# Optimization experiments

Measured on AMD Instinct MI355X. Metric: run time of the kernel, lower is better.

## Reference

```python
import jax, jax.numpy as jnp
import numpy as np

B, TE, TD, D = 8, 2048, 2048, 256

def setup_inputs() -> dict:
    key = jax.random.key(0)
    k1, k2 = jax.random.split(key)
    encoder_outputs = jax.random.normal(k1, (B, TE, D), dtype=jnp.float32)
    decoder_outputs = jax.random.normal(k2, (B, TD, D), dtype=jnp.float32)
    return {"encoder_outputs": encoder_outputs, "decoder_outputs": decoder_outputs}

def reference(encoder_outputs, decoder_outputs):
    # luong_score[b,e,t] = sum_d enc[b,e,d] * dec[b,t,d]   (batch_dot with dec transposed)
    luong_score = jnp.einsum('bed,btd->bet', encoder_outputs, decoder_outputs)
    # softmax over encoder-time axis (axis=1)
    luong_score = jax.nn.softmax(luong_score, axis=1)
    # original does expand_dims + broadcast-multiply + sum over axis=1;
    # same math as a contraction over e: context[b,t,d] = sum_e score[b,e,t]*enc[b,e,d]
    encoder_vector = jnp.einsum('bet,bed->btd', luong_score, encoder_outputs)
    return jnp.concatenate([decoder_outputs, encoder_vector], axis=-1)
```

## Files before the change

kernel.cpp:

```cpp
#include <hip/hip_runtime.h>

typedef _Float16 f16;
typedef _Float16 f16x4 __attribute__((ext_vector_type(4)));
typedef _Float16 f16x8 __attribute__((ext_vector_type(8)));
typedef float    f32x4 __attribute__((ext_vector_type(4)));

#define NB   8
#define TE   2048
#define TD   2048
#define DIM  256
#define NSPLIT 2
#define LOG2E 1.44269504088896340736f

#define AS1(p) ((const __attribute__((address_space(1))) void*)(p))
#define AS3(p) ((__attribute__((address_space(3))) void*)(p))

__global__ __launch_bounds__(256) void prep_kernel(const float* __restrict__ enc,
                                                   f16* __restrict__ ench,
                                                   f16* __restrict__ enct) {
    __shared__ f16 tile[64][72];
    int b  = blockIdx.z;
    int e0 = blockIdx.x * 64;
    int d0 = blockIdx.y * 64;
    int tid = threadIdx.x;
    {
        int e  = tid >> 2;
        int dg = (tid & 3) * 16;
        const float* p = enc + ((size_t)b * TE + e0 + e) * DIM + d0 + dg;
        float4 v0 = *(const float4*)(p);
        float4 v1 = *(const float4*)(p + 4);
        float4 v2 = *(const float4*)(p + 8);
        float4 v3 = *(const float4*)(p + 12);
        f16x8 o0, o1;
        o0[0]=(f16)v0.x; o0[1]=(f16)v0.y; o0[2]=(f16)v0.z; o0[3]=(f16)v0.w;
        o0[4]=(f16)v1.x; o0[5]=(f16)v1.y; o0[6]=(f16)v1.z; o0[7]=(f16)v1.w;
        o1[0]=(f16)v2.x; o1[1]=(f16)v2.y; o1[2]=(f16)v2.z; o1[3]=(f16)v2.w;
        o1[4]=(f16)v3.x; o1[5]=(f16)v3.y; o1[6]=(f16)v3.z; o1[7]=(f16)v3.w;
        *(f16x8*)&tile[e][dg]     = o0;
        *(f16x8*)&tile[e][dg + 8] = o1;
        f16* hp = ench + ((size_t)b * TE + e0 + e) * DIM + d0 + dg;
        *(f16x8*)(hp)     = o0;
        *(f16x8*)(hp + 8) = o1;
    }
    __syncthreads();
    {
        int d  = tid >> 2;
        int eg = (tid & 3) * 16;
        f16x8 o0, o1;
        #pragma unroll
        for (int ii = 0; ii < 8; ii++) o0[ii] = tile[eg + ii][d];
        #pragma unroll
        for (int ii = 0; ii < 8; ii++) o1[ii] = tile[eg + 8 + ii][d];
        f16* qp = enct + ((size_t)b * DIM + d0 + d) * TE + e0 + eg;
        *(f16x8*)(qp)     = o0;
        *(f16x8*)(qp + 8) = o1;
    }
}

#define LDS_NAT0 0
#define LDS_NAT1 16384
#define LDS_TR0  32768
#define LDS_TR1  49152
#define LDS_P    65536

__global__ __launch_bounds__(256, 2) void attn_kernel(
        const float* __restrict__ dec32,
        const f16*  __restrict__ enc_h,
        const f16*  __restrict__ enc_t,
        float* __restrict__ out,
        f16*   __restrict__ ctxp,
        float* __restrict__ m_arr,
        float* __restrict__ l_arr,
        int nsplit) {
    __shared__ char lds[75776];
    const int tid  = threadIdx.x;
    const int lane = tid & 63;
    const int wave = tid >> 6;
    const int th   = wave >> 1;
    const int dh   = wave & 1;
    const int tcol = lane & 15;
    const int q    = lane >> 4;

    int xb, b, z, iters, e_base;
    if (nsplit == NSPLIT) {
        int fid = blockIdx.x + 32 * (blockIdx.y + 8 * blockIdx.z);
        int c = fid & 7, j = fid >> 3;
        xb = j & 31;
        int g = c * 2 + (j >> 5);
        b = g & 7; z = g >> 3;
        iters  = 32;
        e_base = z * 1024;
    } else { xb = blockIdx.x; b = blockIdx.y; z = 0; iters = 64; e_base = 0; }
    const int  t0    = xb * 64;
    const bool heavy = (dh == (xb & 1));

    const f16* enc_b  = enc_h + (size_t)b * TE * DIM;
    const f16* enct_b = enc_t + (size_t)b * DIM * TE;

    const int e00 = tid >> 5, cs0 = tid & 31;
    const int nat_g0 = e00 * DIM + (cs0 ^ (e00 & 7)) * 8;
    const int d00 = tid >> 2, c00 = tid & 3;
    const int tr_g0  = d00 * TE + (c00 ^ ((d00 >> 1) & 3)) * 8;
    const int l0     = wave * 1024;

    #pragma unroll
    for (int i = 0; i < 4; i++)
        __builtin_amdgcn_global_load_lds(AS1(enc_b + (size_t)e_base * DIM + nat_g0 + i * 2048),
                                         AS3(lds + LDS_NAT0 + l0 + i * 4096), 16, 0, 0);
    #pragma unroll
    for (int i = 0; i < 4; i++)
        __builtin_amdgcn_global_load_lds(AS1(enc_b + (size_t)(e_base + 32) * DIM + nat_g0 + i * 2048),
                                         AS3(lds + LDS_NAT1 + l0 + i * 4096), 16, 0, 0);
    #pragma unroll
    for (int i = 0; i < 4; i++)
        __builtin_amdgcn_global_load_lds(AS1(enct_b + e_base + tr_g0 + i * 64 * TE),
                                         AS3(lds + LDS_TR0 + l0 + i * 4096), 16, 0, 0);

    if (nsplit == 1) {
        const float* dp = dec32 + ((size_t)b * TD + t0) * DIM;
        float*       op = out   + ((size_t)b * TD + t0) * 512;
        #pragma unroll
        for (int i = 0; i < 16; i++) {
            int idx = i * 256 + tid;
            int t = idx >> 6, c = idx & 63;
            float4 v = *(const float4*)(dp + t * DIM + c * 4);
            *(float4*)(op + t * 512 + c * 4) = v;
        }
    }

    f16x8 qf[2][8];
    if (heavy) {
        const float* qp = dec32 + ((size_t)b * TD + t0 + th * 32) * DIM;
        #pragma unroll
        for (int tn = 0; tn < 2; tn++)
            #pragma unroll
            for (int ks = 0; ks < 8; ks++) {
                const float* p = qp + (size_t)(tn * 16 + tcol) * DIM + ks * 32 + q * 8;
                float4 u = *(const float4*)(p);
                float4 v = *(const float4*)(p + 4);
                f16x8 o;
                o[0]=(f16)u.x; o[1]=(f16)u.y; o[2]=(f16)u.z; o[3]=(f16)u.w;
                o[4]=(f16)v.x; o[5]=(f16)v.y; o[6]=(f16)v.z; o[7]=(f16)v.w;
                qf[tn][ks] = o;
            }
    }

    f16x8 ones;
    #pragma unroll
    for (int j = 0; j < 8; j++) ones[j] = (f16)1.0f;

    const f32x4 zero4 = {0.f, 0.f, 0.f, 0.f};
    float m_[2] = {-INFINITY, -INFINITY};
    f32x4 lsum[2] = {zero4, zero4};
    f32x4 ctx[8][2];
    #pragma unroll
    for (int dm = 0; dm < 8; dm++)
        #pragma unroll
        for (int tn = 0; tn < 2; tn++) ctx[dm][tn] = zero4;

    const int e7 = tcol & 7;

    __syncthreads();

    for (int it = 0; it < iters; it++) {
        const int natc = (it & 1) ? LDS_NAT1 : LDS_NAT0;
        const int trc  = (it & 1) ? LDS_TR1  : LDS_TR0;
        char* pb = lds + LDS_P + ((it & 1) ? 5120 : 0) + th * 2560;

        if (heavy) {
            f32x4 st[2][2];
            #pragma unroll
            for (int mt = 0; mt < 2; mt++)
                #pragma unroll
                for (int tn = 0; tn < 2; tn++) st[mt][tn] = zero4;
            #pragma unroll
            for (int ks = 0; ks < 8; ks++) {
                #pragma unroll
                for (int mt = 0; mt < 2; mt++) {
                    int e = mt * 16 + tcol;
                    f16x8 af = *(const f16x8*)(lds + natc + e * 512 + (((ks << 2) | q) ^ e7) * 16);
                    #pragma unroll
                    for (int tn = 0; tn < 2; tn++)
                        st[mt][tn] = __builtin_amdgcn_mfma_f32_16x16x32_f16(af, qf[tn][ks], st[mt][tn], 0, 0, 0);
                }
            }
            #pragma unroll
            for (int tn = 0; tn < 2; tn++) {
                float mx = fmaxf(fmaxf(fmaxf(st[0][tn][0], st[0][tn][1]), fmaxf(st[0][tn][2], st[0][tn][3])),
                                 fmaxf(fmaxf(st[1][tn][0], st[1][tn][1]), fmaxf(st[1][tn][2], st[1][tn][3])));
                mx = fmaxf(mx, __shfl_xor(mx, 16, 64));
                mx = fmaxf(mx, __shfl_xor(mx, 32, 64));
                float mn = fmaxf(m_[tn], mx);
                bool bumped = mn > m_[tn];
                float al = __builtin_amdgcn_exp2f((m_[tn] - mn) * LOG2E);
                m_[tn] = mn;
                char* prow = pb + (tn * 16 + tcol) * 80;
                #pragma unroll
                for (int mt = 0; mt < 2; mt++) {
                    f16x4 pv;
                    #pragma unroll
                    for (int r = 0; r < 4; r++)
                        pv[r] = (f16)__builtin_amdgcn_exp2f((st[mt][tn][r] - mn) * LOG2E);
                    *(f16x4*)(prow + mt * 32 + q * 8) = pv;
                }
                if (q == 0) *(float*)(prow + 72) = al;
                if (__any(bumped)) {
                    lsum[tn][0] *= al; lsum[tn][1] *= al; lsum[tn][2] *= al; lsum[tn][3] *= al;
                    #pragma unroll
                    for (int dm = 0; dm < 8; dm++) {
                        ctx[dm][tn][0] *= al; ctx[dm][tn][1] *= al;
                        ctx[dm][tn][2] *= al; ctx[dm][tn][3] *= al;
                    }
                }
            }
        }

        __syncthreads();

        if (it + 1 < iters) {
            const int trn = (it & 1) ? LDS_TR0 : LDS_TR1;
            const int e1  = e_base + (it + 1) * 32;
            #pragma unroll
            for (int i = 0; i < 4; i++)
                __builtin_amdgcn_global_load_lds(AS1(enct_b + e1 + tr_g0 + i * 64 * TE),
                                                 AS3(lds + trn + l0 + i * 4096), 16, 0, 0);
        }
        if (it + 2 < iters) {
            const int e2 = e_base + (it + 2) * 32;
            #pragma unroll
            for (int i = 0; i < 4; i++)
                __builtin_amdgcn_global_load_lds(AS1(enc_b + (size_t)e2 * DIM + nat_g0 + i * 2048),
                                                 AS3(lds + natc + l0 + i * 4096), 16, 0, 0);
        }

        if (!heavy) {
            #pragma unroll
            for (int tn = 0; tn < 2; tn++) {
                float al = *(const float*)(pb + (tn * 16 + tcol) * 80 + 72);
                if (__any(al < 1.0f)) {
                    lsum[tn][0] *= al; lsum[tn][1] *= al; lsum[tn][2] *= al; lsum[tn][3] *= al;
                    #pragma unroll
                    for (int dm = 0; dm < 8; dm++) {
                        ctx[dm][tn][0] *= al; ctx[dm][tn][1] *= al;
                        ctx[dm][tn][2] *= al; ctx[dm][tn][3] *= al;
                    }
                }
            }
        }

        f16x8 pf[2];
        #pragma unroll
        for (int tn = 0; tn < 2; tn++)
            pf[tn] = *(const f16x8*)(pb + (tn * 16 + tcol) * 80 + q * 16);
        #pragma unroll
        for (int tn = 0; tn < 2; tn++)
            lsum[tn] = __builtin_amdgcn_mfma_f32_16x16x32_f16(ones, pf[tn], lsum[tn], 0, 0, 0);
        #pragma unroll
        for (int dm = 0; dm < 8; dm++) {
            int drow = dh * 128 + dm * 16 + tcol;
            f16x8 af = *(const f16x8*)(lds + trc + drow * 64 + (q ^ ((tcol >> 1) & 3)) * 16);
            #pragma unroll
            for (int tn = 0; tn < 2; tn++)
                ctx[dm][tn] = __builtin_amdgcn_mfma_f32_16x16x32_f16(af, pf[tn], ctx[dm][tn], 0, 0, 0);
        }
    }

    if (nsplit > 1) {
        size_t rowbase = (size_t)(z * NB + b) * TD + t0 + th * 32;
        #pragma unroll
        for (int tn = 0; tn < 2; tn++) {
            float inv = 1.0f / lsum[tn][0];
            size_t rb = (rowbase + tn * 16 + tcol) * DIM + dh * 128;
            #pragma unroll
            for (int dm = 0; dm < 8; dm++) {
                f16x4 cv;
                #pragma unroll
                for (int r = 0; r < 4; r++) cv[r] = (f16)(ctx[dm][tn][r] * inv);
                *(f16x4*)(ctxp + rb + dm * 16 + q * 4) = cv;
            }
        }
        if (heavy && lane < 16) {
            int mi = (z * NB + b) * TD + t0 + th * 32 + lane;
            #pragma unroll
            for (int tn = 0; tn < 2; tn++) {
                m_arr[mi + tn * 16] = m_[tn];
                l_arr[mi + tn * 16] = lsum[tn][0];
            }
        }
    } else {
        float* ob = out + ((size_t)b * TD + t0 + th * 32) * 512 + 256 + dh * 128;
        #pragma unroll
        for (int tn = 0; tn < 2; tn++) {
            float inv = 1.0f / lsum[tn][0];
            #pragma unroll
            for (int dm = 0; dm < 8; dm++)
                #pragma unroll
                for (int r = 0; r < 4; r++)
                    ob[(size_t)(tn * 16 + tcol) * 512 + dm * 16 + q * 4 + r] = ctx[dm][tn][r] * inv;
        }
    }
}

__global__ __launch_bounds__(256) void combine_kernel(const float* __restrict__ dec32,
        const f16* __restrict__ ctxp, const float* __restrict__ m_arr,
        const float* __restrict__ l_arr, float* __restrict__ out) {
    int idx  = blockIdx.x * 256 + threadIdx.x;
    int trow = idx >> 5;
    int dg   = (idx & 31) * 8;
    float m0[NSPLIT], l0[NSPLIT], M = -INFINITY;
    #pragma unroll
    for (int s = 0; s < NSPLIT; s++) {
        m0[s] = m_arr[s * (NB * TD) + trow];
        l0[s] = l_arr[s * (NB * TD) + trow];
        M = fmaxf(M, m0[s]);
    }
    float L = 0.f, w[NSPLIT];
    #pragma unroll
    for (int s = 0; s < NSPLIT; s++) {
        w[s] = __builtin_amdgcn_exp2f((m0[s] - M) * LOG2E) * l0[s];
        L += w[s];
    }
    float invL = 1.0f / L;
    float acc[8] = {0.f,0.f,0.f,0.f,0.f,0.f,0.f,0.f};
    #pragma unroll
    for (int s = 0; s < NSPLIT; s++) {
        f16x8 v = *(const f16x8*)(ctxp + ((size_t)s * (NB * TD) + trow) * DIM + dg);
        float ws = w[s] * invL;
        #pragma unroll
        for (int j = 0; j < 8; j++) acc[j] += ws * (float)v[j];
    }
    float4 d0 = *(const float4*)(dec32 + (size_t)trow * DIM + dg);
    float4 d1 = *(const float4*)(dec32 + (size_t)trow * DIM + dg + 4);
    float* ob = out + (size_t)trow * 512;
    *(float4*)(ob + dg)     = d0;
    *(float4*)(ob + dg + 4) = d1;
    float4 c0, c1;
    c0.x=acc[0]; c0.y=acc[1]; c0.z=acc[2]; c0.w=acc[3];
    c1.x=acc[4]; c1.y=acc[5]; c1.z=acc[6]; c1.w=acc[7];
    *(float4*)(ob + 256 + dg)     = c0;
    *(float4*)(ob + 256 + dg + 4) = c1;
}

extern "C" void kernel_launch(void* const* d_in, const int* in_sizes, int n_in,
                              void* d_out, int out_size, void* d_ws, size_t ws_size,
                              hipStream_t stream) {
    (void)in_sizes; (void)n_in;
    const float* enc = (const float*)d_in[0];
    const float* dec = (const float*)d_in[1];
    float* out = (float*)d_out;

    const size_t HB    = (size_t)NB * TE * DIM * 2;
    const size_t CTXPB = (size_t)NSPLIT * NB * TD * DIM * 2;
    const size_t MLB   = (size_t)NSPLIT * NB * TD * 4;
    const size_t NEED2 = 2 * HB + CTXPB + 2 * MLB;
    const size_t NEED1 = 2 * HB;

    if (ws_size < NEED1) {
        hipMemsetAsync(d_out, 0, (size_t)out_size * sizeof(float), stream);
        return;
    }
    int nsplit = (ws_size >= NEED2) ? NSPLIT : 1;

    f16*   enc_h = (f16*)d_ws;
    f16*   enc_t = (f16*)((char*)d_ws + HB);
    f16*   ctxp  = (f16*)((char*)d_ws + 2 * HB);
    float* m_arr = (float*)((char*)d_ws + 2 * HB + CTXPB);
    float* l_arr = (float*)((char*)d_ws + 2 * HB + CTXPB + MLB);

    prep_kernel<<<dim3(32, 4, 8), 256, 0, stream>>>(enc, enc_h, enc_t);
    attn_kernel<<<dim3(32, 8, nsplit), 256, 0, stream>>>(dec, enc_h, enc_t, out,
                                                         ctxp, m_arr, l_arr, nsplit);
    if (nsplit == NSPLIT)
        combine_kernel<<<2048, 256, 0, stream>>>(dec, ctxp, m_arr, l_arr, out);
}
```

Baseline: 150.8 us.

## Drop transposed encoder copy, split work by e-halves, use three-way split

The prep kernel now only converts the encoder to fp16 and no longer writes a transposed copy. The attention kernel stages a single natural-layout tile per step and reads it both for QK and, through strided scalar LDS reads, as the transposed operand for PV. Each wave pair now splits the encoder rows instead of the feature dimension, exchanging row maxima and sums through LDS with an extra barrier per step. The split is raised to three with three blocks per CU, and the nsplit=1 fallback is removed. This saves the transpose traffic and LDS space, at the cost of scalar gathers for PV, extra syncs and more combine traffic.

```diff
diff --git a/kernel.cpp b/kernel.cpp
--- a/kernel.cpp
+++ b/kernel.cpp
@@ -9,127 +9,67 @@
 #define TE   2048
 #define TD   2048
 #define DIM  256
-#define NSPLIT 2
+#define NSPLIT 3
 #define LOG2E 1.44269504088896340736f
 
 #define AS1(p) ((const __attribute__((address_space(1))) void*)(p))
 #define AS3(p) ((__attribute__((address_space(3))) void*)(p))
+#define MFMA16(a,b,c) __builtin_amdgcn_mfma_f32_16x16x32_f16((a),(b),(c),0,0,0)
 
 __global__ __launch_bounds__(256) void prep_kernel(const float* __restrict__ enc,
-                                                   f16* __restrict__ ench,
-                                                   f16* __restrict__ enct) {
-    __shared__ f16 tile[64][72];
-    int b  = blockIdx.z;
-    int e0 = blockIdx.x * 64;
-    int d0 = blockIdx.y * 64;
-    int tid = threadIdx.x;
-    {
-        int e  = tid >> 2;
-        int dg = (tid & 3) * 16;
-        const float* p = enc + ((size_t)b * TE + e0 + e) * DIM + d0 + dg;
-        float4 v0 = *(const float4*)(p);
-        float4 v1 = *(const float4*)(p + 4);
-        float4 v2 = *(const float4*)(p + 8);
-        float4 v3 = *(const float4*)(p + 12);
-        f16x8 o0, o1;
-        o0[0]=(f16)v0.x; o0[1]=(f16)v0.y; o0[2]=(f16)v0.z; o0[3]=(f16)v0.w;
-        o0[4]=(f16)v1.x; o0[5]=(f16)v1.y; o0[6]=(f16)v1.z; o0[7]=(f16)v1.w;
-        o1[0]=(f16)v2.x; o1[1]=(f16)v2.y; o1[2]=(f16)v2.z; o1[3]=(f16)v2.w;
-        o1[4]=(f16)v3.x; o1[5]=(f16)v3.y; o1[6]=(f16)v3.z; o1[7]=(f16)v3.w;
-        *(f16x8*)&tile[e][dg]     = o0;
-        *(f16x8*)&tile[e][dg + 8] = o1;
-        f16* hp = ench + ((size_t)b * TE + e0 + e) * DIM + d0 + dg;
-        *(f16x8*)(hp)     = o0;
-        *(f16x8*)(hp + 8) = o1;
-    }
-    __syncthreads();
-    {
-        int d  = tid >> 2;
-        int eg = (tid & 3) * 16;
-        f16x8 o0, o1;
-        #pragma unroll
-        for (int ii = 0; ii < 8; ii++) o0[ii] = tile[eg + ii][d];
-        #pragma unroll
-        for (int ii = 0; ii < 8; ii++) o1[ii] = tile[eg + 8 + ii][d];
-        f16* qp = enct + ((size_t)b * DIM + d0 + d) * TE + e0 + eg;
-        *(f16x8*)(qp)     = o0;
-        *(f16x8*)(qp + 8) = o1;
-    }
-}
-
-#define LDS_NAT0 0
-#define LDS_NAT1 16384
-#define LDS_TR0  32768
-#define LDS_TR1  49152
-#define LDS_P    65536
-
-__global__ __launch_bounds__(256, 2) void attn_kernel(
+                                                   f16* __restrict__ ench) {
+    size_t i = ((size_t)blockIdx.x * 256 + threadIdx.x) * 8;
+    float4 v0 = *(const float4*)(enc + i);
+    float4 v1 = *(const float4*)(enc + i + 4);
+    f16x8 o;
+    o[0]=(f16)v0.x; o[1]=(f16)v0.y; o[2]=(f16)v0.z; o[3]=(f16)v0.w;
+    o[4]=(f16)v1.x; o[5]=(f16)v1.y; o[6]=(f16)v1.z; o[7]=(f16)v1.w;
+    *(f16x8*)(ench + i) = o;
+}
+
+#define LDS_P  32768
+#define LDS_X  37888
+
+__global__ __launch_bounds__(256, 3) void attn_kernel(
         const float* __restrict__ dec32,
         const f16*  __restrict__ enc_h,
-        const f16*  __restrict__ enc_t,
-        float* __restrict__ out,
         f16*   __restrict__ ctxp,
         float* __restrict__ m_arr,
         float* __restrict__ l_arr,
         int nsplit) {
-    __shared__ char lds[75776];
+    __shared__ __align__(16) char lds[38400];
     const int tid  = threadIdx.x;
     const int lane = tid & 63;
-    const int wave = tid >> 6;
-    const int th   = wave >> 1;
-    const int dh   = wave & 1;
+    const int wv   = tid >> 6;
+    const int th   = wv >> 1;
+    const int eh   = wv & 1;
     const int tcol = lane & 15;
     const int q    = lane >> 4;
 
-    int xb, b, z, iters, e_base;
-    if (nsplit == NSPLIT) {
-        int fid = blockIdx.x + 32 * (blockIdx.y + 8 * blockIdx.z);
-        int c = fid & 7, j = fid >> 3;
-        xb = j & 31;
-        int g = c * 2 + (j >> 5);
-        b = g & 7; z = g >> 3;
-        iters  = 32;
-        e_base = z * 1024;
-    } else { xb = blockIdx.x; b = blockIdx.y; z = 0; iters = 64; e_base = 0; }
-    const int  t0    = xb * 64;
-    const bool heavy = (dh == (xb & 1));
-
-    const f16* enc_b  = enc_h + (size_t)b * TE * DIM;
-    const f16* enct_b = enc_t + (size_t)b * DIM * TE;
-
-    const int e00 = tid >> 5, cs0 = tid & 31;
-    const int nat_g0 = e00 * DIM + (cs0 ^ (e00 & 7)) * 8;
-    const int d00 = tid >> 2, c00 = tid & 3;
-    const int tr_g0  = d00 * TE + (c00 ^ ((d00 >> 1) & 3)) * 8;
-    const int l0     = wave * 1024;
-
-    #pragma unroll
-    for (int i = 0; i < 4; i++)
-        __builtin_amdgcn_global_load_lds(AS1(enc_b + (size_t)e_base * DIM + nat_g0 + i * 2048),
-                                         AS3(lds + LDS_NAT0 + l0 + i * 4096), 16, 0, 0);
-    #pragma unroll
-    for (int i = 0; i < 4; i++)
-        __builtin_amdgcn_global_load_lds(AS1(enc_b + (size_t)(e_base + 32) * DIM + nat_g0 + i * 2048),
-                                         AS3(lds + LDS_NAT1 + l0 + i * 4096), 16, 0, 0);
-    #pragma unroll
-    for (int i = 0; i < 4; i++)
-        __builtin_amdgcn_global_load_lds(AS1(enct_b + e_base + tr_g0 + i * 64 * TE),
-                                         AS3(lds + LDS_TR0 + l0 + i * 4096), 16, 0, 0);
-
-    if (nsplit == 1) {
-        const float* dp = dec32 + ((size_t)b * TD + t0) * DIM;
-        float*       op = out   + ((size_t)b * TD + t0) * 512;
-        #pragma unroll
-        for (int i = 0; i < 16; i++) {
-            int idx = i * 256 + tid;
-            int t = idx >> 6, c = idx & 63;
-            float4 v = *(const float4*)(dp + t * DIM + c * 4);
-            *(float4*)(op + t * 512 + c * 4) = v;
-        }
-    }
+    int fid = blockIdx.x + 32 * (blockIdx.y + 8 * blockIdx.z);
+    const int b  = fid & 7;
+    const int xb = (fid >> 3) & 31;
+    const int z  = fid >> 8;
+    const int t0 = xb * 64;
+    const int tile0 = (64 * z) / nsplit;
+    const int tile1 = (64 * (z + 1)) / nsplit;
+    const int iters = tile1 - tile0;
+
+    const char* encb = (const char*)(enc_h + (size_t)b * TE * DIM);
+
+    const int c0  = wv * 64 + lane;
+    const int e_l = ((c0 >> 7) << 2) | ((c0 >> 1) & 3);
+    const int d_l = (((c0 >> 3) & 15) << 4) | ((c0 & 1) << 3);
+    const int stage_goff = e_l * (DIM * 2) + d_l * 2;
+    char* stage_dst = lds + wv * 1024;
+
+    const int qk_base = (eh * 4 + (tcol >> 2)) * 2048 + (q >> 1) * 128 + (tcol & 3) * 32 + (q & 1) * 16;
+    const int pv_base = q * 4096 + eh * 1024 + tcol * 2;
+    char* pb = lds + LDS_P + th * 2560;
+    float* exch = (float*)(lds + LDS_X);
 
     f16x8 qf[2][8];
-    if (heavy) {
+    {
         const float* qp = dec32 + ((size_t)b * TD + t0 + th * 32) * DIM;
         #pragma unroll
         for (int tn = 0; tn < 2; tn++)
@@ -145,185 +85,148 @@
             }
     }
 
-    f16x8 ones;
-    #pragma unroll
-    for (int j = 0; j < 8; j++) ones[j] = (f16)1.0f;
+    {
+        const char* s = encb + (size_t)tile0 * 16384 + stage_goff;
+        #pragma unroll
+        for (int i = 0; i < 4; i++)
+            __builtin_amdgcn_global_load_lds(AS1(s + i * 4096), AS3(stage_dst + i * 4096), 16, 0, 0);
+    }
 
     const f32x4 zero4 = {0.f, 0.f, 0.f, 0.f};
     float m_[2] = {-INFINITY, -INFINITY};
-    f32x4 lsum[2] = {zero4, zero4};
+    float l_[2] = {0.f, 0.f};
     f32x4 ctx[8][2];
     #pragma unroll
-    for (int dm = 0; dm < 8; dm++)
-        #pragma unroll
-        for (int tn = 0; tn < 2; tn++) ctx[dm][tn] = zero4;
-
-    const int e7 = tcol & 7;
+    for (int dm = 0; dm < 8; dm++) { ctx[dm][0] = zero4; ctx[dm][1] = zero4; }
 
     __syncthreads();
 
-    for (int it = 0; it < iters; it++) {
-        const int natc = (it & 1) ? LDS_NAT1 : LDS_NAT0;
-        const int trc  = (it & 1) ? LDS_TR1  : LDS_TR0;
-        char* pb = lds + LDS_P + ((it & 1) ? 5120 : 0) + th * 2560;
-
-        if (heavy) {
-            f32x4 st[2][2];
-            #pragma unroll
-            for (int mt = 0; mt < 2; mt++)
+    for (int it = 0; it < iters; ++it) {
+        const int nat = (it & 1) << 14;
+        f32x4 st[2] = {zero4, zero4};
+        const char* natp = lds + nat + qk_base;
+        #pragma unroll
+        for (int ks = 0; ks < 8; ks++) {
+            f16x8 af = *(const f16x8*)(natp + ks * 256);
+            st[0] = MFMA16(af, qf[0][ks], st[0]);
+            st[1] = MFMA16(af, qf[1][ks], st[1]);
+        }
+        float mx[2];
+        #pragma unroll
+        for (int tn = 0; tn < 2; tn++) {
+            float m0 = fmaxf(fmaxf(st[tn][0], st[tn][1]), fmaxf(st[tn][2], st[tn][3]));
+            m0 = fmaxf(m0, __shfl_xor(m0, 16, 64));
+            m0 = fmaxf(m0, __shfl_xor(m0, 32, 64));
+            mx[tn] = m0;
+        }
+        if (q == 0) { exch[wv * 32 + tcol] = mx[0]; exch[wv * 32 + 16 + tcol] = mx[1]; }
+        __syncthreads();
+        if (it + 1 < iters) {
+            const char* s = encb + (size_t)(tile0 + it + 1) * 16384 + stage_goff;
+            char* dd = stage_dst + (((it + 1) & 1) << 14);
+            #pragma unroll
+            for (int i = 0; i < 4; i++)
+                __builtin_amdgcn_global_load_lds(AS1(s + i * 4096), AS3(dd + i * 4096), 16, 0, 0);
+        }
+        bool anyb = false;
+        float al[2], s4v[2];
+        #pragma unroll
+        for (int tn = 0; tn < 2; tn++) {
+            float ox = exch[(wv ^ 1) * 32 + tn * 16 + tcol];
+            float mn = fmaxf(m_[tn], fmaxf(mx[tn], ox));
+            al[tn] = __builtin_amdgcn_exp2f((m_[tn] - mn) * LOG2E);
+            anyb = anyb || (mn > m_[tn]);
+            m_[tn] = mn;
+            f16x4 pv;
+            #pragma unroll
+            for (int r = 0; r < 4; r++)
+                pv[r] = (f16)__builtin_amdgcn_exp2f((st[tn][r] - mn) * LOG2E);
+            *(f16x4*)(pb + (tn * 16 + tcol) * 80 + eh * 32 + q * 8) = pv;
+            float s4 = ((float)pv[0] + (float)pv[1]) + ((float)pv[2] + (float)pv[3]);
+            s4 += __shfl_xor(s4, 16, 64);
+            s4 += __shfl_xor(s4, 32, 64);
+            s4v[tn] = s4;
+        }
+        if (__any(anyb)) {
+            #pragma unroll
+            for (int tn = 0; tn < 2; tn++) {
+                l_[tn] *= al[tn];
                 #pragma unroll
-                for (int tn = 0; tn < 2; tn++) st[mt][tn] = zero4;
-            #pragma unroll
-            for (int ks = 0; ks < 8; ks++) {
-                #pragma unroll
-                for (int mt = 0; mt < 2; mt++) {
-                    int e = mt * 16 + tcol;
-                    f16x8 af = *(const f16x8*)(lds + natc + e * 512 + (((ks << 2) | q) ^ e7) * 16);
-                    #pragma unroll
-                    for (int tn = 0; tn < 2; tn++)
-                        st[mt][tn] = __builtin_amdgcn_mfma_f32_16x16x32_f16(af, qf[tn][ks], st[mt][tn], 0, 0, 0);
+                for (int dm = 0; dm < 8; dm++) {
+                    ctx[dm][tn][0] *= al[tn]; ctx[dm][tn][1] *= al[tn];
+                    ctx[dm][tn][2] *= al[tn]; ctx[dm][tn][3] *= al[tn];
                 }
             }
-            #pragma unroll
-            for (int tn = 0; tn < 2; tn++) {
-                float mx = fmaxf(fmaxf(fmaxf(st[0][tn][0], st[0][tn][1]), fmaxf(st[0][tn][2], st[0][tn][3])),
-                                 fmaxf(fmaxf(st[1][tn][0], st[1][tn][1]), fmaxf(st[1][tn][2], st[1][tn][3])));
-                mx = fmaxf(mx, __shfl_xor(mx, 16, 64));
-                mx = fmaxf(mx, __shfl_xor(mx, 32, 64));
-                float mn = fmaxf(m_[tn], mx);
-                bool bumped = mn > m_[tn];
-                float al = __builtin_amdgcn_exp2f((m_[tn] - mn) * LOG2E);
-                m_[tn] = mn;
-                char* prow = pb + (tn * 16 + tcol) * 80;
-                #pragma unroll
-                for (int mt = 0; mt < 2; mt++) {
-                    f16x4 pv;
-                    #pragma unroll
-                    for (int r = 0; r < 4; r++)
-                        pv[r] = (f16)__builtin_amdgcn_exp2f((st[mt][tn][r] - mn) * LOG2E);
-                    *(f16x4*)(prow + mt * 32 + q * 8) = pv;
-                }
-                if (q == 0) *(float*)(prow + 72) = al;
-                if (__any(bumped)) {
-                    lsum[tn][0] *= al; lsum[tn][1] *= al; lsum[tn][2] *= al; lsum[tn][3] *= al;
-                    #pragma unroll
-                    for (int dm = 0; dm < 8; dm++) {
-                        ctx[dm][tn][0] *= al; ctx[dm][tn][1] *= al;
-                        ctx[dm][tn][2] *= al; ctx[dm][tn][3] *= al;
-                    }
-                }
+        }
+        l_[0] += s4v[0]; l_[1] += s4v[1];
+        __syncthreads();
+        f16x8 pf0 = *(const f16x8*)(pb + tcol * 80 + q * 16);
+        f16x8 pf1 = *(const f16x8*)(pb + (16 + tcol) * 80 + q * 16);
+        const char* trp = lds + nat + pv_base;
+        #pragma unroll
+        for (int dm = 0; dm < 8; dm++) {
+            const char* base = trp + dm * 128;
+            f16x8 af;
+            #pragma unroll
+            for (int j = 0; j < 4; j++) {
+                af[j]     = *(const f16*)(base + j * 32);
+                af[j + 4] = *(const f16*)(base + 2048 + j * 32);
             }
-        }
-
-        __syncthreads();
-
-        if (it + 1 < iters) {
-            const int trn = (it & 1) ? LDS_TR0 : LDS_TR1;
-            const int e1  = e_base + (it + 1) * 32;
-            #pragma unroll
-            for (int i = 0; i < 4; i++)
-                __builtin_amdgcn_global_load_lds(AS1(enct_b + e1 + tr_g0 + i * 64 * TE),
-                                                 AS3(lds + trn + l0 + i * 4096), 16, 0, 0);
-        }
-        if (it + 2 < iters) {
-            const int e2 = e_base + (it + 2) * 32;
-            #pragma unroll
-            for (int i = 0; i < 4; i++)
-                __builtin_amdgcn_global_load_lds(AS1(enc_b + (size_t)e2 * DIM + nat_g0 + i * 2048),
-                                                 AS3(lds + natc + l0 + i * 4096), 16, 0, 0);
-        }
-
-        if (!heavy) {
-            #pragma unroll
-            for (int tn = 0; tn < 2; tn++) {
-                float al = *(const float*)(pb + (tn * 16 + tcol) * 80 + 72);
-                if (__any(al < 1.0f)) {
-                    lsum[tn][0] *= al; lsum[tn][1] *= al; lsum[tn][2] *= al; lsum[tn][3] *= al;
-                    #pragma unroll
-                    for (int dm = 0; dm < 8; dm++) {
-                        ctx[dm][tn][0] *= al; ctx[dm][tn][1] *= al;
-                        ctx[dm][tn][2] *= al; ctx[dm][tn][3] *= al;
-                    }
-                }
-            }
-        }
-
-        f16x8 pf[2];
-        #pragma unroll
-        for (int tn = 0; tn < 2; tn++)
-            pf[tn] = *(const f16x8*)(pb + (tn * 16 + tcol) * 80 + q * 16);
-        #pragma unroll
-        for (int tn = 0; tn < 2; tn++)
-            lsum[tn] = __builtin_amdgcn_mfma_f32_16x16x32_f16(ones, pf[tn], lsum[tn], 0, 0, 0);
+            ctx[dm][0] = MFMA16(af, pf0, ctx[dm][0]);
+            ctx[dm][1] = MFMA16(af, pf1, ctx[dm][1]);
+        }
+    }
+
+    if (q == 0) { exch[wv * 32 + tcol] = l_[0]; exch[wv * 32 + 16 + tcol] = l_[1]; }
+    __syncthreads();
+    float lt[2];
+    lt[0] = l_[0] + exch[(wv ^ 1) * 32 + tcol];
+    lt[1] = l_[1] + exch[(wv ^ 1) * 32 + 16 + tcol];
+    size_t row0 = (size_t)(z * NB + b) * TD + t0 + th * 32;
+    #pragma unroll
+    for (int tn = 0; tn < 2; tn++) {
+        float inv = 1.0f / lt[tn];
+        size_t rb = (row0 + tn * 16 + tcol) * DIM + eh * 128;
         #pragma unroll
         for (int dm = 0; dm < 8; dm++) {
-            int drow = dh * 128 + dm * 16 + tcol;
-            f16x8 af = *(const f16x8*)(lds + trc + drow * 64 + (q ^ ((tcol >> 1) & 3)) * 16);
-            #pragma unroll
-            for (int tn = 0; tn < 2; tn++)
-                ctx[dm][tn] = __builtin_amdgcn_mfma_f32_16x16x32_f16(af, pf[tn], ctx[dm][tn], 0, 0, 0);
-        }
-    }
-
-    if (nsplit > 1) {
-        size_t rowbase = (size_t)(z * NB + b) * TD + t0 + th * 32;
-        #pragma unroll
-        for (int tn = 0; tn < 2; tn++) {
-            float inv = 1.0f / lsum[tn][0];
-            size_t rb = (rowbase + tn * 16 + tcol) * DIM + dh * 128;
-            #pragma unroll
-            for (int dm = 0; dm < 8; dm++) {
-                f16x4 cv;
-                #pragma unroll
-                for (int r = 0; r < 4; r++) cv[r] = (f16)(ctx[dm][tn][r] * inv);
-                *(f16x4*)(ctxp + rb + dm * 16 + q * 4) = cv;
-            }
-        }
-        if (heavy && lane < 16) {
-            int mi = (z * NB + b) * TD + t0 + th * 32 + lane;
-            #pragma unroll
-            for (int tn = 0; tn < 2; tn++) {
-                m_arr[mi + tn * 16] = m_[tn];
-                l_arr[mi + tn * 16] = lsum[tn][0];
-            }
-        }
-    } else {
-        float* ob = out + ((size_t)b * TD + t0 + th * 32) * 512 + 256 + dh * 128;
-        #pragma unroll
-        for (int tn = 0; tn < 2; tn++) {
-            float inv = 1.0f / lsum[tn][0];
-            #pragma unroll
-            for (int dm = 0; dm < 8; dm++)
-                #pragma unroll
-                for (int r = 0; r < 4; r++)
-                    ob[(size_t)(tn * 16 + tcol) * 512 + dm * 16 + q * 4 + r] = ctx[dm][tn][r] * inv;
-        }
+            f16x4 cv;
+            #pragma unroll
+            for (int r = 0; r < 4; r++) cv[r] = (f16)(ctx[dm][tn][r] * inv);
+            *(f16x4*)(ctxp + rb + dm * 16 + q * 4) = cv;
+        }
+    }
+    if (eh == 0 && q == 0) {
+        int mi = (z * NB + b) * TD + t0 + th * 32 + tcol;
+        m_arr[mi]      = m_[0];
+        m_arr[mi + 16] = m_[1];
+        l_arr[mi]      = lt[0];
+        l_arr[mi + 16] = lt[1];
     }
 }
 
 __global__ __launch_bounds__(256) void combine_kernel(const float* __restrict__ dec32,
         const f16* __restrict__ ctxp, const float* __restrict__ m_arr,
-        const float* __restrict__ l_arr, float* __restrict__ out) {
+        const float* __restrict__ l_arr, float* __restrict__ out, int nsplit) {
     int idx  = blockIdx.x * 256 + threadIdx.x;
     int trow = idx >> 5;
     int dg   = (idx & 31) * 8;
     float m0[NSPLIT], l0[NSPLIT], M = -INFINITY;
     #pragma unroll
-    for (int s = 0; s < NSPLIT; s++) {
+    for (int s = 0; s < NSPLIT; s++) if (s < nsplit) {
         m0[s] = m_arr[s * (NB * TD) + trow];
         l0[s] = l_arr[s * (NB * TD) + trow];
         M = fmaxf(M, m0[s]);
     }
     float L = 0.f, w[NSPLIT];
     #pragma unroll
-    for (int s = 0; s < NSPLIT; s++) {
+    for (int s = 0; s < NSPLIT; s++) if (s < nsplit) {
         w[s] = __builtin_amdgcn_exp2f((m0[s] - M) * LOG2E) * l0[s];
         L += w[s];
     }
     float invL = 1.0f / L;
     float acc[8] = {0.f,0.f,0.f,0.f,0.f,0.f,0.f,0.f};
     #pragma unroll
-    for (int s = 0; s < NSPLIT; s++) {
+    for (int s = 0; s < NSPLIT; s++) if (s < nsplit) {
         f16x8 v = *(const f16x8*)(ctxp + ((size_t)s * (NB * TD) + trow) * DIM + dg);
         float ws = w[s] * invL;
         #pragma unroll
@@ -349,27 +252,21 @@
     const float* dec = (const float*)d_in[1];
     float* out = (float*)d_out;
 
-    const size_t HB    = (size_t)NB * TE * DIM * 2;
-    const size_t CTXPB = (size_t)NSPLIT * NB * TD * DIM * 2;
-    const size_t MLB   = (size_t)NSPLIT * NB * TD * 4;
-    const size_t NEED2 = 2 * HB + CTXPB + 2 * MLB;
-    const size_t NEED1 = 2 * HB;
-
-    if (ws_size < NEED1) {
-        hipMemsetAsync(d_out, 0, (size_t)out_size * sizeof(float), stream);
-        return;
-    }
-    int nsplit = (ws_size >= NEED2) ? NSPLIT : 1;
-
-    f16*   enc_h = (f16*)d_ws;
-    f16*   enc_t = (f16*)((char*)d_ws + HB);
-    f16*   ctxp  = (f16*)((char*)d_ws + 2 * HB);
-    float* m_arr = (float*)((char*)d_ws + 2 * HB + CTXPB);
-    float* l_arr = (float*)((char*)d_ws + 2 * HB + CTXPB + MLB);
-
-    prep_kernel<<<dim3(32, 4, 8), 256, 0, stream>>>(enc, enc_h, enc_t);
-    attn_kernel<<<dim3(32, 8, nsplit), 256, 0, stream>>>(dec, enc_h, enc_t, out,
-                                                         ctxp, m_arr, l_arr, nsplit);
-    if (nsplit == NSPLIT)
-        combine_kernel<<<2048, 256, 0, stream>>>(dec, ctxp, m_arr, l_arr, out);
-}
+    const size_t MLB = (size_t)NSPLIT * NB * TD * 4;
+    const size_t HB  = (size_t)NB * TE * DIM * 2;
+    const size_t CSL = (size_t)NB * TD * DIM * 2;
+
+    float* m_arr = (float*)d_ws;
+    float* l_arr = (float*)((char*)d_ws + MLB);
+    f16*   ench  = (f16*)((char*)d_ws + 2 * MLB);
+    f16*   ctxp  = (f16*)((char*)d_ws + 2 * MLB + HB);
+
+    int nsplit;
+    if      (ws_size >= 2 * MLB + HB + 3 * CSL) nsplit = 3;
+    else if (ws_size >= 2 * MLB + HB + 2 * CSL) nsplit = 2;
+    else { hipMemsetAsync(d_out, 0, (size_t)out_size * sizeof(float), stream); return; }
+
+    prep_kernel<<<2048, 256, 0, stream>>>(enc, ench);
+    attn_kernel<<<dim3(32, 8, nsplit), 256, 0, stream>>>(dec, ench, ctxp, m_arr, l_arr, nsplit);
+    combine_kernel<<<2048, 256, 0, stream>>>(dec, ctxp, m_arr, l_arr, out, nsplit);
+}
```

Result: slower. 167.4 us (+11.0%).
